# Kernel optimization log

Hardware: AMD Instinct MI355X
Metric: run time of the kernel (lower is better)

The kernel has to match this reference:

```python
import jax, jax.numpy as jnp
import numpy as np

N, E = 30000, 300000          # nodes, edges
IN, HID, OUT, H = 128, 256, 64, 4  # feature dims, GAT heads
NEG_SLOPE = 0.2
BN_EPS = 1e-5


def setup_inputs() -> dict:
    key = jax.random.key(0)
    ks = jax.random.split(key, 18)
    rn = lambda k, sh, sc: (jax.random.normal(k, sh, jnp.float32) * sc)
    return {
        "x": rn(ks[0], (N, IN), 1.0),
        "edge_index": jax.random.randint(ks[1], (2, E), 0, N, dtype=jnp.int64),
        # SAGEConv 1: lin_l (aggregated neighbors, with bias) + lin_r (root)
        "W1l": rn(ks[2], (IN, HID), IN ** -0.5),
        "b1l": jnp.zeros((HID,), jnp.float32),
        "W1r": rn(ks[3], (IN, HID), IN ** -0.5),
        # SAGEConv 2
        "W2l": rn(ks[4], (HID, OUT), HID ** -0.5),
        "b2l": jnp.zeros((OUT,), jnp.float32),
        "W2r": rn(ks[5], (HID, OUT), HID ** -0.5),
        # BatchNorms
        "g1": jnp.ones((HID,), jnp.float32),
        "be1": jnp.zeros((HID,), jnp.float32),
        "g2": jnp.ones((OUT,), jnp.float32),
        "be2": jnp.zeros((OUT,), jnp.float32),
        # GATConv: heads=4, concat=False (mean over heads)
        "Wg": rn(ks[6], (OUT, H * OUT), OUT ** -0.5),
        "att_src": rn(ks[7], (H, OUT), OUT ** -0.5),
        "att_dst": rn(ks[8], (H, OUT), OUT ** -0.5),
        "bg": jnp.zeros((OUT,), jnp.float32),
    }


def _forward(x, W1l, b1l, W1r, W2l, b2l, W2r, g1, be1, g2, be2,
             Wg, att_src, att_dst, bg, edge_index):
    src, dst = edge_index[0], edge_index[1]

    def sage(x, Wl, bl, Wr):
        # PyG SAGEConv: lin_l(mean_{j in N(i)} x_j) + lin_r(x_i)
        msg = jax.ops.segment_sum(x[src], dst, num_segments=N)       # [N, D]
        deg = jax.ops.segment_sum(jnp.ones((E, 1), x.dtype), dst, num_segments=N)
        agg = msg / jnp.maximum(deg, 1.0)
        return agg @ Wl + bl + x @ Wr

    def bn(x, g, b):  # batch-statistics BatchNorm1d (training-mode math)
        mu = x.mean(0)
        var = x.var(0)
        return g * (x - mu) * jax.lax.rsqrt(var + BN_EPS) + b

    x = jax.nn.relu(bn(sage(x, W1l, b1l, W1r), g1, be1))   # [N, HID]
    x = jax.nn.relu(bn(sage(x, W2l, b2l, W2r), g2, be2))   # [N, OUT]

    # GATConv with default add_self_loops=True
    loop = jnp.arange(N, dtype=src.dtype)
    s2 = jnp.concatenate([src, loop])
    d2 = jnp.concatenate([dst, loop])
    xp = (x @ Wg).reshape(N, H, OUT)                       # [N, H, D]
    a_src = (xp * att_src).sum(-1)                         # [N, H]
    a_dst = (xp * att_dst).sum(-1)                         # [N, H]
    e = jax.nn.leaky_relu(a_src[s2] + a_dst[d2], NEG_SLOPE)  # [E+N, H]
    # segment softmax over incoming edges per target node
    m = jax.ops.segment_max(e, d2, num_segments=N)
    ee = jnp.exp(e - m[d2])
    denom = jax.ops.segment_sum(ee, d2, num_segments=N)
    alpha = ee / denom[d2]                                 # [E+N, H]
    out = jax.ops.segment_sum(alpha[:, :, None] * xp[s2], d2, num_segments=N)
    out = out.mean(axis=1) + bg                            # concat=False -> head mean
    out = jax.nn.relu(out)
    return out.mean(axis=0, keepdims=True)                 # [1, OUT]


def reference(x, edge_index, W1l, b1l, W1r, W2l, b2l, W2r,
              g1, be1, g2, be2, Wg, att_src, att_dst, bg):
    return _forward(x, W1l, b1l, W1r, W2l, b2l, W2r, g1, be1, g2, be2,
                    Wg, att_src, att_dst, bg, edge_index)
```

## Files before the change

### kernel.cpp

```cpp
#include <hip/hip_runtime.h>
#include <stdint.h>

#define N_NODES 30000
#define N_EDGES 300000
#define BN_EPS  1e-5f
#define NEG_SLOPE 0.2f

typedef __attribute__((ext_vector_type(8))) short          s16x8;
typedef __attribute__((ext_vector_type(8))) unsigned short u16x8;
typedef __attribute__((ext_vector_type(4))) float          f32x4;

__device__ __forceinline__ float b2f(unsigned int u) { return __uint_as_float(u << 16); }
__device__ __forceinline__ unsigned int f2b(float f) {
    unsigned int u = __float_as_uint(f);
    return (u + 0x7fffu + ((u >> 16) & 1u)) >> 16;
}
__device__ __forceinline__ unsigned int f2q(float f) {
    unsigned int s = (__float_as_uint(f) >> 31) << 7;
    float af = fminf(fabsf(f), 448.f);
    if (af < 0.015625f) {
        int m = (int)rintf(af * 512.f);
        return s | (unsigned int)m;
    }
    unsigned int b = __float_as_uint(af);
    b += 0x7FFFFu + ((b >> 20) & 1u);
    unsigned int e = (b >> 23) - 120u;
    unsigned int m = (b >> 20) & 7u;
    if (e > 15u) { e = 15u; m = 6u; }
    return s | (e << 3) | m;
}
__device__ __forceinline__ float q2f(unsigned int u) {
    unsigned int em = u & 0x7f;
    float nrm = __uint_as_float((((em >> 3) + 120u) << 23) | ((em & 7u) << 20));
    float den = (float)em * 0.001953125f;
    float mag = (em >= 8u) ? nrm : den;
    return (u & 0x80u) ? -mag : mag;
}
__device__ __forceinline__ float lrelu(float a) { return fmaxf(a, NEG_SLOPE * a); }

__global__ void k_prep(int* __restrict__ cnt, float* __restrict__ stats, float* __restrict__ outz,
                       const float* __restrict__ x, unsigned short* __restrict__ xb,
                       unsigned char* __restrict__ xq,
                       const float* __restrict__ W1l, const float* __restrict__ W1r,
                       const float* __restrict__ W2l, const float* __restrict__ W2r,
                       const float* __restrict__ Wg,
                       unsigned short* __restrict__ t1l, unsigned short* __restrict__ t1r,
                       unsigned short* __restrict__ t2l, unsigned short* __restrict__ t2r,
                       unsigned short* __restrict__ btf,
                       const float* __restrict__ att_src, const float* __restrict__ att_dst,
                       float* __restrict__ vsrc, float* __restrict__ vdst) {
    int b = blockIdx.x, tid = threadIdx.x;
    if (b < 118) {
        int i = b * 256 + tid;
        if (i < N_NODES) cnt[i] = 0;
        if (i < 3072) stats[i] = 0.f;
        if (b == 0 && tid < 64) outz[tid] = 0.f;
    } else if (b < 1118) {
        for (int i = (b - 118) * 256 + tid; i < N_NODES * 128 / 4; i += 256000) {
            float4 v = ((const float4*)x)[i];
            unsigned int lo = f2b(v.x) | (f2b(v.y) << 16);
            unsigned int hi = f2b(v.z) | (f2b(v.w) << 16);
            ((uint2*)xb)[i] = make_uint2(lo, hi);
            unsigned int q = f2q(v.x) | (f2q(v.y) << 8) | (f2q(v.z) << 16) | (f2q(v.w) << 24);
            ((unsigned int*)xq)[i] = q;
        }
    } else if (b < 1566) {
        int i = (b - 1118) * 256 + tid;
        if (i >= 114688) return;
        if (i >= 98304) {
            int j = i - 98304;
            int n = j >> 8, r = j & 255;
            int h = r >> 6, k = r & 63;
            btf[j] = f2b(Wg[k * 256 + h * 64 + n] * 0.25f);
            return;
        }
        const float* S; unsigned short* D; int K, NN, off;
        if (i < 32768)      { S = W1l; D = t1l; K = 128; NN = 256; off = 0; }
        else if (i < 65536) { S = W1r; D = t1r; K = 128; NN = 256; off = 32768; }
        else if (i < 81920) { S = W2l; D = t2l; K = 256; NN = 64;  off = 65536; }
        else                { S = W2r; D = t2r; K = 256; NN = 64;  off = 81920; }
        int j = i - off;
        int k = j / NN, n = j % NN;
        D[n * K + k] = f2b(S[j]);
    } else {
        int h = tid >> 6, k = tid & 63;
        float s = 0.f, d = 0.f;
        for (int dd = 0; dd < 64; ++dd) {
            float w = Wg[k * 256 + h * 64 + dd];
            s += w * att_src[h * 64 + dd];
            d += w * att_dst[h * 64 + dd];
        }
        vsrc[h * 64 + k] = s;
        vdst[h * 64 + k] = d;
    }
}

__global__ void k_count(const int* __restrict__ dst, int* __restrict__ cnt) {
    int e = blockIdx.x * 256 + threadIdx.x;
    if (e < N_EDGES) atomicAdd(&cnt[dst[e]], 1);
}

__global__ void k_scan1(const int* __restrict__ cnt, int* __restrict__ rowptr, int* __restrict__ bsums) {
    __shared__ int s[256];
    int tid = threadIdx.x;
    int idx = blockIdx.x * 256 + tid;
    int val = (idx < N_NODES) ? cnt[idx] : 0;
    s[tid] = val; __syncthreads();
    for (int o = 1; o < 256; o <<= 1) {
        int add = (tid >= o) ? s[tid - o] : 0;
        __syncthreads();
        s[tid] += add;
        __syncthreads();
    }
    if (idx < N_NODES) rowptr[idx] = s[tid] - val;
    if (tid == 255) bsums[blockIdx.x] = s[255];
}

__global__ void k_scan3(int* __restrict__ rowptr, const int* __restrict__ bsums, int* __restrict__ cnt) {
    __shared__ int ls[128];
    int tid = threadIdx.x;
    if (tid < 128) ls[tid] = (tid < 118) ? bsums[tid] : 0;
    __syncthreads();
    for (int o = 1; o < 128; o <<= 1) {
        int add = (tid < 128 && tid >= o) ? ls[tid - o] : 0;
        __syncthreads();
        if (tid < 128) ls[tid] += add;
        __syncthreads();
    }
    int ex = (blockIdx.x == 0) ? 0 : ls[blockIdx.x - 1];
    int idx = blockIdx.x * 256 + tid;
    if (idx < N_NODES) { rowptr[idx] += ex; cnt[idx] = 0; }
    if (idx == 0) rowptr[N_NODES] = N_EDGES;
}

__global__ void k_fill(const int* __restrict__ srcA, const int* __restrict__ dstA,
                       const int* __restrict__ rowptr, int* __restrict__ cnt, int* __restrict__ col) {
    int e = blockIdx.x * 256 + threadIdx.x;
    if (e < N_EDGES) {
        int d = dstA[e];
        int pos = rowptr[d] + atomicAdd(&cnt[d], 1);
        col[pos] = srcA[e];
    }
}

__global__ void __launch_bounds__(256) k_sage_agg_q(const unsigned char* __restrict__ Xq,
                                                    const int* __restrict__ rowptr,
                                                    const int* __restrict__ col,
                                                    unsigned short* __restrict__ out) {
    int lane = threadIdx.x & 63;
    int i = (blockIdx.x << 2) + (threadIdx.x >> 6);
    if (i >= N_NODES) return;
    int eg = lane >> 4, fq = lane & 15;
    int b = rowptr[i], e = rowptr[i + 1];
    float a[8] = {};
    int p = b;
    int i0 = p + eg, i1 = p + 4 + eg;
    int j0 = (i0 < e) ? col[i0] : i; float m0 = (i0 < e) ? 1.f : 0.f;
    int j1 = (i1 < e) ? col[i1] : i; float m1 = (i1 < e) ? 1.f : 0.f;
    while (p < e) {
        int i2 = p + 8 + eg, i3 = p + 12 + eg;
        int j2 = (i2 < e) ? col[i2] : i; float m2 = (i2 < e) ? 1.f : 0.f;
        int j3 = (i3 < e) ? col[i3] : i; float m3 = (i3 < e) ? 1.f : 0.f;
        uint2 g0 = *(const uint2*)(Xq + (size_t)j0 * 128 + fq * 8);
        uint2 g1 = *(const uint2*)(Xq + (size_t)j1 * 128 + fq * 8);
        #pragma unroll
        for (int q = 0; q < 4; ++q) {
            a[q]     += m0 * q2f((g0.x >> (q * 8)) & 0xffu) + m1 * q2f((g1.x >> (q * 8)) & 0xffu);
            a[4 + q] += m0 * q2f((g0.y >> (q * 8)) & 0xffu) + m1 * q2f((g1.y >> (q * 8)) & 0xffu);
        }
        j0 = j2; m0 = m2; j1 = j3; m1 = m3; p += 8;
    }
    #pragma unroll
    for (int q = 0; q < 8; ++q) {
        a[q] += __shfl_xor(a[q], 16);
        a[q] += __shfl_xor(a[q], 32);
    }
    if (lane < 16) {
        float inv = 1.f / fmaxf((float)(e - b), 1.f);
        uint4 o;
        o.x = f2b(a[0] * inv) | (f2b(a[1] * inv) << 16);
        o.y = f2b(a[2] * inv) | (f2b(a[3] * inv) << 16);
        o.z = f2b(a[4] * inv) | (f2b(a[5] * inv) << 16);
        o.w = f2b(a[6] * inv) | (f2b(a[7] * inv) << 16);
        *(uint4*)(out + (size_t)i * 128 + fq * 8) = o;
    }
}

template<int OUTM, bool BN_A, bool STATS>
__global__ void __launch_bounds__(256) k_mgemm(const unsigned short* __restrict__ A1,
                                               const unsigned short* __restrict__ Bt1, int K1,
                                               const unsigned short* __restrict__ A2,
                                               const unsigned short* __restrict__ Bt2, int K2,
                                               const float* __restrict__ bias,
                                               void* __restrict__ Cv,
                                               unsigned char* __restrict__ Czq,
                                               unsigned short* __restrict__ Cr2,
                                               int M, int NN,
                                               const float* __restrict__ bn_sum,
                                               const float* __restrict__ bn_sq,
                                               const float* __restrict__ bn_g,
                                               const float* __restrict__ bn_be,
                                               float* __restrict__ stS, float* __restrict__ stQ) {
    __shared__ unsigned short As[64 * 32];
    __shared__ unsigned short Bs[64 * 32];
    __shared__ float bnAl[256], bnBl[256];
    int tid = threadIdx.x;
    int w = tid >> 6, l = tid & 63;
    int mBase = blockIdx.x * 64, nBase = blockIdx.y * 64;
    f32x4 acc[4] = {};

    if constexpr (BN_A) {
        float su = bn_sum[tid] + bn_sum[256 + tid] + bn_sum[512 + tid] + bn_sum[768 + tid];
        float sq = bn_sq[tid] + bn_sq[256 + tid] + bn_sq[512 + tid] + bn_sq[768 + tid];
        float mu = su * (1.f / N_NODES);
        float var = sq * (1.f / N_NODES) - mu * mu;
        float a = bn_g[tid] * rsqrtf(var + BN_EPS);
        bnAl[tid] = a;
        bnBl[tid] = bn_be[tid] - a * mu;
        __syncthreads();
    }

    auto lds_off = [](int row, int col_bf16) -> int {
        return (row * 64 + col_bf16 * 2) ^ ((row & 7) << 4);
    };
    int srow = tid >> 2;
    int schunk = (tid & 3) << 3;
    int s_w_off = lds_off(srow, schunk);
    int kgrp = (l >> 4) << 3;
    int a_off = lds_off(w * 16 + (l & 15), kgrp);
    int b_off[4];
    #pragma unroll
    for (int c = 0; c < 4; ++c) b_off[c] = lds_off(c * 16 + (l & 15), kgrp);

    for (int pair = 0; pair < 2; ++pair) {
        const unsigned short* A  = pair ? A2 : A1;
        const unsigned short* Bt = pair ? Bt2 : Bt1;
        int K = pair ? K2 : K1;
        if (K == 0) break;
        for (int k0 = 0; k0 < K; k0 += 32) {
            u16x8 av = {};
            int arow = mBase + srow;
            if (arow < M) {
                av = *(const u16x8*)&A[(size_t)arow * K + k0 + schunk];
                if constexpr (BN_A) {
                    const float* pa = &bnAl[k0 + schunk];
                    const float* pb = &bnBl[k0 + schunk];
                    #pragma unroll
                    for (int e2 = 0; e2 < 8; ++e2) {
                        float f = fmaxf(b2f(av[e2]) * pa[e2] + pb[e2], 0.f);
                        av[e2] = (unsigned short)f2b(f);
                    }
                }
            }
            u16x8 bv = *(const u16x8*)&Bt[(size_t)(nBase + srow) * K + k0 + schunk];
            *(u16x8*)((char*)As + s_w_off) = av;
            *(u16x8*)((char*)Bs + s_w_off) = bv;
            __syncthreads();
            s16x8 a = *(const s16x8*)((const char*)As + a_off);
            #pragma unroll
            for (int c = 0; c < 4; ++c) {
                s16x8 bfr = *(const s16x8*)((const char*)Bs + b_off[c]);
                acc[c] = __builtin_amdgcn_mfma_f32_16x16x32_bf16(a, bfr, acc[c], 0, 0, 0);
            }
            __syncthreads();
        }
    }

    float* lst = (float*)As;
    if constexpr (STATS) {
        if (tid < 128) lst[tid] = 0.f;
        __syncthreads();
    }
    int colb = l & 15;
    int rbase = (l >> 4) << 2;
    #pragma unroll
    for (int c = 0; c < 4; ++c) {
        int gcol = nBase + c * 16 + colb;
        float bi = bias ? bias[gcol] : 0.f;
        float s_ = 0.f, q_ = 0.f;
        #pragma unroll
        for (int r = 0; r < 4; ++r) {
            int grow = mBase + w * 16 + rbase + r;
            if (grow < M) {
                float v = acc[c][r] + bi;
                if constexpr (OUTM == 1) {
                    ((unsigned short*)Cv)[(size_t)grow * NN + gcol] = (unsigned short)f2b(v);
                } else {
                    if (gcol < 64) Czq[(size_t)grow * 64 + gcol] = (unsigned char)f2q(v);
                    else           Cr2[(size_t)grow * 64 + gcol - 64] = (unsigned short)f2b(v);
                }
                if constexpr (STATS) { s_ += v; q_ += v * v; }
            }
        }
        if constexpr (STATS) {
            s_ += __shfl_xor(s_, 16); s_ += __shfl_xor(s_, 32);
            q_ += __shfl_xor(q_, 16); q_ += __shfl_xor(q_, 32);
            if (l < 16) {
                atomicAdd(&lst[c * 16 + l], s_);
                atomicAdd(&lst[64 + c * 16 + l], q_);
            }
        }
    }
    if constexpr (STATS) {
        __syncthreads();
        int rep = (blockIdx.x & 3) * 256;
        if (tid < 64) {
            atomicAdd(&stS[rep + nBase + tid], lst[tid]);
            atomicAdd(&stQ[rep + nBase + tid], lst[64 + tid]);
        }
    }
}

__global__ void __launch_bounds__(256) k_mgemm_mean(const unsigned short* __restrict__ A,
                                                    const unsigned short* __restrict__ Bt,
                                                    const float* __restrict__ bg,
                                                    float* __restrict__ out, int M) {
    __shared__ unsigned short As[64 * 32];
    __shared__ unsigned short Bs[64 * 32];
    __shared__ float lds_cols[64];
    int tid = threadIdx.x;
    int w = tid >> 6, l = tid & 63;
    int mBase = blockIdx.x * 64;
    if (tid < 64) lds_cols[tid] = 0.f;
    f32x4 acc[4] = {};

    auto lds_off = [](int row, int col_bf16) -> int {
        return (row * 64 + col_bf16 * 2) ^ ((row & 7) << 4);
    };
    int srow = tid >> 2;
    int schunk = (tid & 3) << 3;
    int s_w_off = lds_off(srow, schunk);
    int kgrp = (l >> 4) << 3;
    int a_off = lds_off(w * 16 + (l & 15), kgrp);
    int b_off[4];
    #pragma unroll
    for (int c = 0; c < 4; ++c) b_off[c] = lds_off(c * 16 + (l & 15), kgrp);

    const int K = 256;
    for (int k0 = 0; k0 < K; k0 += 32) {
        u16x8 av = {};
        int arow = mBase + srow;
        if (arow < M) av = *(const u16x8*)&A[(size_t)arow * K + k0 + schunk];
        u16x8 bv = *(const u16x8*)&Bt[(size_t)srow * K + k0 + schunk];
        *(u16x8*)((char*)As + s_w_off) = av;
        *(u16x8*)((char*)Bs + s_w_off) = bv;
        __syncthreads();
        s16x8 a = *(const s16x8*)((const char*)As + a_off);
        #pragma unroll
        for (int c = 0; c < 4; ++c) {
            s16x8 bfr = *(const s16x8*)((const char*)Bs + b_off[c]);
            acc[c] = __builtin_amdgcn_mfma_f32_16x16x32_bf16(a, bfr, acc[c], 0, 0, 0);
        }
        __syncthreads();
    }

    int colb = l & 15;
    int rbase = (l >> 4) << 2;
    #pragma unroll
    for (int c = 0; c < 4; ++c) {
        int gcol = c * 16 + colb;
        float bi = bg[gcol];
        float sc = 0.f;
        #pragma unroll
        for (int r = 0; r < 4; ++r) {
            int grow = mBase + w * 16 + rbase + r;
            if (grow < M) sc += fmaxf(acc[c][r] + bi, 0.f);
        }
        sc += __shfl_xor(sc, 16);
        sc += __shfl_xor(sc, 32);
        if (l < 16) atomicAdd(&lds_cols[c * 16 + l], sc);
    }
    __syncthreads();
    if (tid < 64) atomicAdd(out + tid, lds_cols[tid] * (1.f / N_NODES));
}

__global__ void __launch_bounds__(256) k_sage_add(const unsigned char* __restrict__ zq,
                                                  const unsigned short* __restrict__ r2,
                                                  const int* __restrict__ rowptr,
                                                  const int* __restrict__ col,
                                                  const float* __restrict__ b2l,
                                                  unsigned short* __restrict__ h2,
                                                  float* __restrict__ stS, float* __restrict__ stQ) {
    __shared__ float ls[128];
    int tid = threadIdx.x;
    if (tid < 128) ls[tid] = 0.f;
    __syncthreads();
    int lane = tid & 63;
    int wid = tid >> 6;
    int eg = lane >> 4, fq = lane & 15;
    float4 blv = ((const float4*)b2l)[fq];
    float sa[4] = {}, qa[4] = {};
    for (int i = blockIdx.x * 4 + wid; i < N_NODES; i += gridDim.x * 4) {
        int b = rowptr[i], e = rowptr[i + 1];
        float a[4] = {};
        int p = b;
        int i0 = p + eg, i1 = p + 4 + eg;
        int j0 = (i0 < e) ? col[i0] : i; float m0 = (i0 < e) ? 1.f : 0.f;
        int j1 = (i1 < e) ? col[i1] : i; float m1 = (i1 < e) ? 1.f : 0.f;
        while (p < e) {
            int i2 = p + 8 + eg, i3 = p + 12 + eg;
            int j2 = (i2 < e) ? col[i2] : i; float m2 = (i2 < e) ? 1.f : 0.f;
            int j3 = (i3 < e) ? col[i3] : i; float m3 = (i3 < e) ? 1.f : 0.f;
            unsigned int g0 = *(const unsigned int*)(zq + (size_t)j0 * 64 + fq * 4);
            unsigned int g1 = *(const unsigned int*)(zq + (size_t)j1 * 64 + fq * 4);
            #pragma unroll
            for (int q = 0; q < 4; ++q)
                a[q] += m0 * q2f((g0 >> (q * 8)) & 0xffu) + m1 * q2f((g1 >> (q * 8)) & 0xffu);
            j0 = j2; m0 = m2; j1 = j3; m1 = m3; p += 8;
        }
        #pragma unroll
        for (int q = 0; q < 4; ++q) {
            a[q] += __shfl_xor(a[q], 16);
            a[q] += __shfl_xor(a[q], 32);
        }
        if (lane < 16) {
            float inv = 1.f / fmaxf((float)(e - b), 1.f);
            uint2 rr = *(const uint2*)(r2 + (size_t)i * 64 + fq * 4);
            float v0 = a[0] * inv + blv.x + b2f(rr.x & 0xffffu);
            float v1 = a[1] * inv + blv.y + b2f(rr.x >> 16);
            float v2 = a[2] * inv + blv.z + b2f(rr.y & 0xffffu);
            float v3 = a[3] * inv + blv.w + b2f(rr.y >> 16);
            uint2 o;
            o.x = f2b(v0) | (f2b(v1) << 16);
            o.y = f2b(v2) | (f2b(v3) << 16);
            *(uint2*)(h2 + (size_t)i * 64 + fq * 4) = o;
            sa[0] += v0; qa[0] += v0 * v0;
            sa[1] += v1; qa[1] += v1 * v1;
            sa[2] += v2; qa[2] += v2 * v2;
            sa[3] += v3; qa[3] += v3 * v3;
        }
    }
    if (lane < 16) {
        #pragma unroll
        for (int q = 0; q < 4; ++q) {
            atomicAdd(&ls[fq * 4 + q], sa[q]);
            atomicAdd(&ls[64 + fq * 4 + q], qa[q]);
        }
    }
    __syncthreads();
    int rep = (blockIdx.x & 3) * 64;
    if (tid < 64) {
        atomicAdd(&stS[rep + tid], ls[tid]);
        atomicAdd(&stQ[rep + tid], ls[64 + tid]);
    }
}

__global__ void __launch_bounds__(256) k_attn2(const unsigned short* __restrict__ h2,
                                               const float* __restrict__ sum2,
                                               const float* __restrict__ sq2,
                                               const float* __restrict__ g2,
                                               const float* __restrict__ be2,
                                               const float* __restrict__ vsrc,
                                               const float* __restrict__ vdst,
                                               unsigned char* __restrict__ h2q,
                                               float* __restrict__ att) {
    int tid = threadIdx.x;
    int lane = tid & 63;
    int wid = tid >> 6;
    float su = sum2[lane] + sum2[64 + lane] + sum2[128 + lane] + sum2[192 + lane];
    float sq = sq2[lane] + sq2[64 + lane] + sq2[128 + lane] + sq2[192 + lane];
    float mu = su * (1.f / N_NODES);
    float var = sq * (1.f / N_NODES) - mu * mu;
    float a2 = g2[lane] * rsqrtf(var + BN_EPS);
    float b2v = be2[lane] - a2 * mu;
    float vs0 = vsrc[lane], vs1 = vsrc[64 + lane], vs2 = vsrc[128 + lane], vs3 = vsrc[192 + lane];
    float vd0 = vdst[lane], vd1 = vdst[64 + lane], vd2 = vdst[128 + lane], vd3 = vdst[192 + lane];
    for (int i = blockIdx.x * 4 + wid; i < N_NODES; i += gridDim.x * 4) {
        float v = fmaxf(b2f(__builtin_nontemporal_load(h2 + (size_t)i * 64 + lane)) * a2 + b2v, 0.f);
        h2q[(size_t)i * 64 + lane] = (unsigned char)f2q(v);
        float s0 = v * vs0, s1 = v * vs1, s2 = v * vs2, s3 = v * vs3;
        float d0 = v * vd0, d1 = v * vd1, d2 = v * vd2, d3 = v * vd3;
        #pragma unroll
        for (int o = 32; o; o >>= 1) {
            s0 += __shfl_xor(s0, o); s1 += __shfl_xor(s1, o);
            s2 += __shfl_xor(s2, o); s3 += __shfl_xor(s3, o);
            d0 += __shfl_xor(d0, o); d1 += __shfl_xor(d1, o);
            d2 += __shfl_xor(d2, o); d3 += __shfl_xor(d3, o);
        }
        if (lane == 0) {
            float4* ap = (float4*)(att + (size_t)i * 8);
            ap[0] = make_float4(s0, s1, s2, s3);
            ap[1] = make_float4(d0, d1, d2, d3);
        }
    }
}

__global__ void __launch_bounds__(256) k_gat2(const unsigned char* __restrict__ h2q,
                                              const float* __restrict__ att,
                                              const int* __restrict__ rowptr,
                                              const int* __restrict__ col,
                                              unsigned short* __restrict__ oagg) {
    int tid = threadIdx.x;
    int lane = tid & 63;
    int eg = lane >> 4, fq = lane & 15;
    int gw = (blockIdx.x << 2) + (tid >> 6);
    int stride = gridDim.x << 2;
    for (int i = gw; i < N_NODES; i += stride) {
        int b = rowptr[i], e = rowptr[i + 1];
        float4 ai = *(const float4*)(att + (size_t)i * 8);
        float4 ad = *(const float4*)(att + (size_t)i * 8 + 4);
        unsigned int hvg = *(const unsigned int*)(h2q + (size_t)i * 64 + fq * 4);
        float hv[4];
        #pragma unroll
        for (int q = 0; q < 4; ++q) hv[q] = q2f((hvg >> (q * 8)) & 0xffu);
        float wself0 = __expf(lrelu(ai.x + ad.x));
        float wself1 = __expf(lrelu(ai.y + ad.y));
        float wself2 = __expf(lrelu(ai.z + ad.z));
        float wself3 = __expf(lrelu(ai.w + ad.w));
        float sg = (eg == 0) ? 1.f : 0.f;
        float s[4] = { sg * wself0, sg * wself1, sg * wself2, sg * wself3 };
        float acc[4][4];
        #pragma unroll
        for (int q = 0; q < 4; ++q) {
            acc[0][q] = s[0] * hv[q];
            acc[1][q] = s[1] * hv[q];
            acc[2][q] = s[2] * hv[q];
            acc[3][q] = s[3] * hv[q];
        }
        int p = b;
        int i0 = p + eg, i1 = p + 4 + eg;
        int j0 = (i0 < e) ? col[i0] : i; float m0 = (i0 < e) ? 1.f : 0.f;
        int j1 = (i1 < e) ? col[i1] : i; float m1 = (i1 < e) ? 1.f : 0.f;
        while (p < e) {
            int i2 = p + 8 + eg, i3 = p + 12 + eg;
            int j2 = (i2 < e) ? col[i2] : i; float m2 = (i2 < e) ? 1.f : 0.f;
            int j3 = (i3 < e) ? col[i3] : i; float m3 = (i3 < e) ? 1.f : 0.f;
            float4 ap0 = *(const float4*)(att + (size_t)j0 * 8);
            float4 ap1 = *(const float4*)(att + (size_t)j1 * 8);
            unsigned int g0 = *(const unsigned int*)(h2q + (size_t)j0 * 64 + fq * 4);
            unsigned int g1 = *(const unsigned int*)(h2q + (size_t)j1 * 64 + fq * 4);
            float w00 = m0 * __expf(lrelu(ap0.x + ad.x));
            float w01 = m0 * __expf(lrelu(ap0.y + ad.y));
            float w02 = m0 * __expf(lrelu(ap0.z + ad.z));
            float w03 = m0 * __expf(lrelu(ap0.w + ad.w));
            float w10 = m1 * __expf(lrelu(ap1.x + ad.x));
            float w11 = m1 * __expf(lrelu(ap1.y + ad.y));
            float w12 = m1 * __expf(lrelu(ap1.z + ad.z));
            float w13 = m1 * __expf(lrelu(ap1.w + ad.w));
            s[0] += w00 + w10; s[1] += w01 + w11; s[2] += w02 + w12; s[3] += w03 + w13;
            #pragma unroll
            for (int q = 0; q < 4; ++q) {
                float x0 = q2f((g0 >> (q * 8)) & 0xffu);
                float x1 = q2f((g1 >> (q * 8)) & 0xffu);
                acc[0][q] = fmaf(w00, x0, fmaf(w10, x1, acc[0][q]));
                acc[1][q] = fmaf(w01, x0, fmaf(w11, x1, acc[1][q]));
                acc[2][q] = fmaf(w02, x0, fmaf(w12, x1, acc[2][q]));
                acc[3][q] = fmaf(w03, x0, fmaf(w13, x1, acc[3][q]));
            }
            j0 = j2; m0 = m2; j1 = j3; m1 = m3; p += 8;
        }
        #pragma unroll
        for (int h = 0; h < 4; ++h) {
            s[h] += __shfl_xor(s[h], 16);
            s[h] += __shfl_xor(s[h], 32);
            #pragma unroll
            for (int q = 0; q < 4; ++q) {
                acc[h][q] += __shfl_xor(acc[h][q], 16);
                acc[h][q] += __shfl_xor(acc[h][q], 32);
            }
        }
        if (lane < 16) {
            unsigned short* op = oagg + (size_t)i * 256 + fq * 4;
            #pragma unroll
            for (int h = 0; h < 4; ++h) {
                float r = 1.f / s[h];
                uint2 o;
                o.x = f2b(acc[h][0] * r) | (f2b(acc[h][1] * r) << 16);
                o.y = f2b(acc[h][2] * r) | (f2b(acc[h][3] * r) << 16);
                *(uint2*)(op + h * 64) = o;
            }
        }
    }
}

extern "C" void kernel_launch(void* const* d_in, const int* in_sizes, int n_in,
                              void* d_out, int out_size, void* d_ws, size_t ws_size,
                              hipStream_t stream) {
    const float* x       = (const float*)d_in[0];
    const int*   ei      = (const int*)d_in[1];
    const float* W1l     = (const float*)d_in[2];
    const float* b1l     = (const float*)d_in[3];
    const float* W1r     = (const float*)d_in[4];
    const float* W2l     = (const float*)d_in[5];
    const float* b2l     = (const float*)d_in[6];
    const float* W2r     = (const float*)d_in[7];
    const float* g1      = (const float*)d_in[8];
    const float* be1     = (const float*)d_in[9];
    const float* g2      = (const float*)d_in[10];
    const float* be2     = (const float*)d_in[11];
    const float* Wg      = (const float*)d_in[12];
    const float* att_src = (const float*)d_in[13];
    const float* att_dst = (const float*)d_in[14];
    const float* bg      = (const float*)d_in[15];
    float* out = (float*)d_out;

    char* p = (char*)d_ws;
    auto alloc = [&](size_t bytes) -> char* {
        char* q = p;
        p += (bytes + 255) & ~(size_t)255;
        return q;
    };
    int*   cnt    = (int*)alloc((size_t)N_NODES * 4);
    float* stats  = (float*)alloc(3072 * 4);
    int*   rowptr = (int*)alloc((size_t)(N_NODES + 1) * 4);
    int*   bsums  = (int*)alloc(256 * 4);
    int*   col    = (int*)alloc((size_t)N_EDGES * 4);
    unsigned short* xb  = (unsigned short*)alloc((size_t)N_NODES * 128 * 2);
    unsigned char*  xq  = (unsigned char*)alloc((size_t)N_NODES * 128);
    unsigned short* agg1b = (unsigned short*)alloc((size_t)N_NODES * 128 * 2);
    unsigned short* h1b = (unsigned short*)alloc((size_t)N_NODES * 256 * 2);
    unsigned char*  zq  = (unsigned char*)alloc((size_t)N_NODES * 64);
    unsigned short* r2  = (unsigned short*)alloc((size_t)N_NODES * 64 * 2);
    unsigned short* h2  = (unsigned short*)alloc((size_t)N_NODES * 64 * 2);
    unsigned char*  h2q = (unsigned char*)alloc((size_t)N_NODES * 64);
    float* att  = (float*)alloc((size_t)N_NODES * 8 * 4);
    unsigned short* w1lt = (unsigned short*)alloc(128 * 256 * 2);
    unsigned short* w1rt = (unsigned short*)alloc(128 * 256 * 2);
    unsigned short* w2lt = (unsigned short*)alloc(256 * 64 * 2);
    unsigned short* w2rt = (unsigned short*)alloc(256 * 64 * 2);
    unsigned short* btf  = (unsigned short*)alloc(64 * 256 * 2);

    unsigned short* oagg = xb;

    float* sum1 = stats;
    float* sq1  = stats + 1024;
    float* sum2 = stats + 2048;
    float* sq2  = stats + 2304;
    float* vsrc = stats + 2560;
    float* vdst = stats + 2816;

    const int* srcA = ei;
    const int* dstA = ei + N_EDGES;

    k_prep<<<1567, 256, 0, stream>>>(cnt, stats, out, x, xb, xq, W1l, W1r, W2l, W2r, Wg,
                                     w1lt, w1rt, w2lt, w2rt, btf, att_src, att_dst, vsrc, vdst);
    k_count<<<1172, 256, 0, stream>>>(dstA, cnt);
    k_scan1<<<118, 256, 0, stream>>>(cnt, rowptr, bsums);
    k_scan3<<<118, 256, 0, stream>>>(rowptr, bsums, cnt);
    k_fill<<<1172, 256, 0, stream>>>(srcA, dstA, rowptr, cnt, col);

    k_sage_agg_q<<<7500, 256, 0, stream>>>(xq, rowptr, col, agg1b);
    k_mgemm<1, false, true><<<dim3(469, 4), 256, 0, stream>>>(
        agg1b, w1lt, 128, xb, w1rt, 128, b1l, h1b, nullptr, nullptr, N_NODES, 256,
        nullptr, nullptr, nullptr, nullptr, sum1, sq1);

    k_mgemm<2, true, false><<<dim3(469, 2), 256, 0, stream>>>(
        h1b, w2lt, 256, nullptr, nullptr, 0, nullptr, nullptr, zq, r2, N_NODES, 128,
        sum1, sq1, g1, be1, nullptr, nullptr);
    k_sage_add<<<1875, 256, 0, stream>>>(zq, r2, rowptr, col, b2l, h2, sum2, sq2);

    k_attn2<<<1875, 256, 0, stream>>>(h2, sum2, sq2, g2, be2, vsrc, vdst, h2q, att);
    k_gat2<<<2048, 256, 0, stream>>>(h2q, att, rowptr, col, oagg);
    k_mgemm_mean<<<469, 256, 0, stream>>>(oagg, btf, bg, out, N_NODES);
}
```

Before: 203.6 us.

## Precompute per-edge GAT attention weights in a separate kernel before aggregation

Adds a dst array in CSR order during fill and a new edge-parallel kernel that computes the exp(leaky_relu) attention weights once per edge into a buffer. Self-loop weights are now computed in k_attn2. k_gat2 reads these precomputed weights sequentially instead of gathering att rows and computing exp redundantly across the 16 lanes of each edge group. This removes redundant transcendental work and random att gathers from the aggregation loop, at the cost of an extra kernel launch and a 4.8 MB write plus read of the weight buffer.

New measurement: 206.6 us. About the same (+1.5%).

```diff
diff --git a/kernel.cpp b/kernel.cpp
--- a/kernel.cpp
+++ b/kernel.cpp
@@ -134,12 +134,14 @@
 }
 
 __global__ void k_fill(const int* __restrict__ srcA, const int* __restrict__ dstA,
-                       const int* __restrict__ rowptr, int* __restrict__ cnt, int* __restrict__ col) {
+                       const int* __restrict__ rowptr, int* __restrict__ cnt,
+                       int* __restrict__ col, int* __restrict__ dstp) {
     int e = blockIdx.x * 256 + threadIdx.x;
     if (e < N_EDGES) {
         int d = dstA[e];
         int pos = rowptr[d] + atomicAdd(&cnt[d], 1);
         col[pos] = srcA[e];
+        dstp[pos] = d;
     }
 }
 
@@ -453,7 +455,8 @@
                                                const float* __restrict__ vsrc,
                                                const float* __restrict__ vdst,
                                                unsigned char* __restrict__ h2q,
-                                               float* __restrict__ att) {
+                                               float* __restrict__ att,
+                                               float4* __restrict__ wself) {
     int tid = threadIdx.x;
     int lane = tid & 63;
     int wid = tid >> 6;
@@ -481,12 +484,32 @@
             float4* ap = (float4*)(att + (size_t)i * 8);
             ap[0] = make_float4(s0, s1, s2, s3);
             ap[1] = make_float4(d0, d1, d2, d3);
-        }
-    }
+            wself[i] = make_float4(__expf(lrelu(s0 + d0)), __expf(lrelu(s1 + d1)),
+                                   __expf(lrelu(s2 + d2)), __expf(lrelu(s3 + d3)));
+        }
+    }
+}
+
+__global__ void __launch_bounds__(256) k_edgeexp(const int* __restrict__ col,
+                                                 const int* __restrict__ dstp,
+                                                 const float* __restrict__ att,
+                                                 float4* __restrict__ wbuf) {
+    int p = blockIdx.x * 256 + threadIdx.x;
+    if (p >= N_EDGES) return;
+    int j = col[p], d = dstp[p];
+    float4 as = *(const float4*)(att + (size_t)j * 8);
+    float4 ad = *(const float4*)(att + (size_t)d * 8 + 4);
+    float4 w;
+    w.x = __expf(lrelu(as.x + ad.x));
+    w.y = __expf(lrelu(as.y + ad.y));
+    w.z = __expf(lrelu(as.z + ad.z));
+    w.w = __expf(lrelu(as.w + ad.w));
+    wbuf[p] = w;
 }
 
 __global__ void __launch_bounds__(256) k_gat2(const unsigned char* __restrict__ h2q,
-                                              const float* __restrict__ att,
+                                              const float4* __restrict__ wbuf,
+                                              const float4* __restrict__ wself,
                                               const int* __restrict__ rowptr,
                                               const int* __restrict__ col,
                                               unsigned short* __restrict__ oagg) {
@@ -497,46 +520,32 @@
     int stride = gridDim.x << 2;
     for (int i = gw; i < N_NODES; i += stride) {
         int b = rowptr[i], e = rowptr[i + 1];
-        float4 ai = *(const float4*)(att + (size_t)i * 8);
-        float4 ad = *(const float4*)(att + (size_t)i * 8 + 4);
         unsigned int hvg = *(const unsigned int*)(h2q + (size_t)i * 64 + fq * 4);
         float hv[4];
         #pragma unroll
         for (int q = 0; q < 4; ++q) hv[q] = q2f((hvg >> (q * 8)) & 0xffu);
-        float wself0 = __expf(lrelu(ai.x + ad.x));
-        float wself1 = __expf(lrelu(ai.y + ad.y));
-        float wself2 = __expf(lrelu(ai.z + ad.z));
-        float wself3 = __expf(lrelu(ai.w + ad.w));
+        float4 ws = wself[i];
         float sg = (eg == 0) ? 1.f : 0.f;
-        float s[4] = { sg * wself0, sg * wself1, sg * wself2, sg * wself3 };
+        float s[4] = { sg * ws.x, sg * ws.y, sg * ws.z, sg * ws.w };
         float acc[4][4];
         #pragma unroll
-        for (int q = 0; q < 4; ++q) {
-            acc[0][q] = s[0] * hv[q];
-            acc[1][q] = s[1] * hv[q];
-            acc[2][q] = s[2] * hv[q];
-            acc[3][q] = s[3] * hv[q];
-        }
+        for (int h = 0; h < 4; ++h)
+            #pragma unroll
+            for (int q = 0; q < 4; ++q) acc[h][q] = s[h] * hv[q];
         int p = b;
         int i0 = p + eg, i1 = p + 4 + eg;
-        int j0 = (i0 < e) ? col[i0] : i; float m0 = (i0 < e) ? 1.f : 0.f;
-        int j1 = (i1 < e) ? col[i1] : i; float m1 = (i1 < e) ? 1.f : 0.f;
+        int j0 = (i0 < e) ? col[i0] : i; int p0 = (i0 < e) ? i0 : 0; float m0 = (i0 < e) ? 1.f : 0.f;
+        int j1 = (i1 < e) ? col[i1] : i; int p1 = (i1 < e) ? i1 : 0; float m1 = (i1 < e) ? 1.f : 0.f;
         while (p < e) {
             int i2 = p + 8 + eg, i3 = p + 12 + eg;
-            int j2 = (i2 < e) ? col[i2] : i; float m2 = (i2 < e) ? 1.f : 0.f;
-            int j3 = (i3 < e) ? col[i3] : i; float m3 = (i3 < e) ? 1.f : 0.f;
-            float4 ap0 = *(const float4*)(att + (size_t)j0 * 8);
-            float4 ap1 = *(const float4*)(att + (size_t)j1 * 8);
+            int j2 = (i2 < e) ? col[i2] : i; int p2 = (i2 < e) ? i2 : 0; float m2 = (i2 < e) ? 1.f : 0.f;
+            int j3 = (i3 < e) ? col[i3] : i; int p3 = (i3 < e) ? i3 : 0; float m3 = (i3 < e) ? 1.f : 0.f;
+            float4 wb0 = wbuf[p0];
+            float4 wb1 = wbuf[p1];
             unsigned int g0 = *(const unsigned int*)(h2q + (size_t)j0 * 64 + fq * 4);
             unsigned int g1 = *(const unsigned int*)(h2q + (size_t)j1 * 64 + fq * 4);
-            float w00 = m0 * __expf(lrelu(ap0.x + ad.x));
-            float w01 = m0 * __expf(lrelu(ap0.y + ad.y));
-            float w02 = m0 * __expf(lrelu(ap0.z + ad.z));
-            float w03 = m0 * __expf(lrelu(ap0.w + ad.w));
-            float w10 = m1 * __expf(lrelu(ap1.x + ad.x));
-            float w11 = m1 * __expf(lrelu(ap1.y + ad.y));
-            float w12 = m1 * __expf(lrelu(ap1.z + ad.z));
-            float w13 = m1 * __expf(lrelu(ap1.w + ad.w));
+            float w00 = m0 * wb0.x, w01 = m0 * wb0.y, w02 = m0 * wb0.z, w03 = m0 * wb0.w;
+            float w10 = m1 * wb1.x, w11 = m1 * wb1.y, w12 = m1 * wb1.z, w13 = m1 * wb1.w;
             s[0] += w00 + w10; s[1] += w01 + w11; s[2] += w02 + w12; s[3] += w03 + w13;
             #pragma unroll
             for (int q = 0; q < 4; ++q) {
@@ -547,7 +556,7 @@
                 acc[2][q] = fmaf(w02, x0, fmaf(w12, x1, acc[2][q]));
                 acc[3][q] = fmaf(w03, x0, fmaf(w13, x1, acc[3][q]));
             }
-            j0 = j2; m0 = m2; j1 = j3; m1 = m3; p += 8;
+            j0 = j2; p0 = p2; m0 = m2; j1 = j3; p1 = p3; m1 = m3; p += 8;
         }
         #pragma unroll
         for (int h = 0; h < 4; ++h) {
@@ -605,6 +614,7 @@
     int*   rowptr = (int*)alloc((size_t)(N_NODES + 1) * 4);
     int*   bsums  = (int*)alloc(256 * 4);
     int*   col    = (int*)alloc((size_t)N_EDGES * 4);
+    int*   dstp   = (int*)alloc((size_t)N_EDGES * 4);
     unsigned short* xb  = (unsigned short*)alloc((size_t)N_NODES * 128 * 2);
     unsigned char*  xq  = (unsigned char*)alloc((size_t)N_NODES * 128);
     unsigned short* agg1b = (unsigned short*)alloc((size_t)N_NODES * 128 * 2);
@@ -614,6 +624,8 @@
     unsigned short* h2  = (unsigned short*)alloc((size_t)N_NODES * 64 * 2);
     unsigned char*  h2q = (unsigned char*)alloc((size_t)N_NODES * 64);
     float* att  = (float*)alloc((size_t)N_NODES * 8 * 4);
+    float4* wself = (float4*)alloc((size_t)N_NODES * 16);
+    float4* wbuf  = (float4*)alloc((size_t)N_EDGES * 16);
     unsigned short* w1lt = (unsigned short*)alloc(128 * 256 * 2);
     unsigned short* w1rt = (unsigned short*)alloc(128 * 256 * 2);
     unsigned short* w2lt = (unsigned short*)alloc(256 * 64 * 2);
@@ -637,7 +649,7 @@
     k_count<<<1172, 256, 0, stream>>>(dstA, cnt);
     k_scan1<<<118, 256, 0, stream>>>(cnt, rowptr, bsums);
     k_scan3<<<118, 256, 0, stream>>>(rowptr, bsums, cnt);
-    k_fill<<<1172, 256, 0, stream>>>(srcA, dstA, rowptr, cnt, col);
+    k_fill<<<1172, 256, 0, stream>>>(srcA, dstA, rowptr, cnt, col, dstp);
 
     k_sage_agg_q<<<7500, 256, 0, stream>>>(xq, rowptr, col, agg1b);
     k_mgemm<1, false, true><<<dim3(469, 4), 256, 0, stream>>>(
@@ -649,7 +661,8 @@
         sum1, sq1, g1, be1, nullptr, nullptr);
     k_sage_add<<<1875, 256, 0, stream>>>(zq, r2, rowptr, col, b2l, h2, sum2, sq2);
 
-    k_attn2<<<1875, 256, 0, stream>>>(h2, sum2, sq2, g2, be2, vsrc, vdst, h2q, att);
-    k_gat2<<<2048, 256, 0, stream>>>(h2q, att, rowptr, col, oagg);
+    k_attn2<<<1875, 256, 0, stream>>>(h2, sum2, sq2, g2, be2, vsrc, vdst, h2q, att, wself);
+    k_edgeexp<<<1172, 256, 0, stream>>>(col, dstp, att, wbuf);
+    k_gat2<<<2048, 256, 0, stream>>>(h2q, wbuf, wself, rowptr, col, oagg);
     k_mgemm_mean<<<469, 256, 0, stream>>>(oagg, btf, bg, out, N_NODES);
 }
```
